# Performance work log

Hardware: AMD Instinct MI355X
Metric: run time of the kernel (lower is better)

Reference implementation:

```python
import jax, jax.numpy as jnp
import numpy as np

B = 524288
NF, NH1, NH21, NH22, NCLS = 5, 128, 32, 32, 1


def setup_inputs() -> dict:
    key = jax.random.key(0)
    ks = jax.random.split(key, 12)
    s = 0.05
    return {
        "x": jax.random.normal(ks[0], (B, NF), dtype=jnp.float32),
        "mean": jnp.zeros((NF,), dtype=jnp.float32),
        "std": jnp.ones((NF,), dtype=jnp.float32),
        "W1": jax.random.normal(ks[1], (NH1, NF), dtype=jnp.float32) * s,
        "b1": jax.random.normal(ks[2], (NH1,), dtype=jnp.float32) * s,
        "W21": jax.random.normal(ks[3], (NH21, NH1), dtype=jnp.float32) * s,
        "b21": jax.random.normal(ks[4], (NH21,), dtype=jnp.float32) * s,
        "W22": jax.random.normal(ks[5], (NH22, NH1), dtype=jnp.float32) * s,
        "b22": jax.random.normal(ks[6], (NH22,), dtype=jnp.float32) * s,
        "W31": jax.random.normal(ks[7], (NCLS, NH21), dtype=jnp.float32) * s,
        "b31": jax.random.normal(ks[8], (NCLS,), dtype=jnp.float32) * s,
        "W32": jax.random.normal(ks[9], (NCLS, NH22), dtype=jnp.float32) * s,
        "b32": jax.random.normal(ks[10], (NCLS,), dtype=jnp.float32) * s,
    }


def reference(x, mean, std, W1, b1, W21, b21, W22, b22, W31, b31, W32, b32):
    # de-normalized state used to build the CBF inequality
    x0 = x * std + mean  # [B, 5]
    h1 = jax.nn.relu(x @ W1.T + b1)         # [B, 128]  (bn=False path)
    x21 = jax.nn.relu(h1 @ W21.T + b21)     # [B, 32]
    x22 = jax.nn.relu(h1 @ W22.T + b22)     # [B, 32]
    x31 = x21 @ W31.T + b31                 # [B, 1]  QP linear term p
    x32 = 4.0 * jax.nn.sigmoid(x22 @ W32.T + b32)  # [B, 1]  learned penalty
    # h for the single inequality 1.8*u <= h
    h = (x0[:, 1] - x0[:, 3])[:, None] + x32 * (x0[:, 0] - x0[:, 2] - 1.8 * x0[:, 3])[:, None]
    # Closed-form 1-D QP: min 0.5 u^2 + x31*u  s.t. 1.8 u <= h
    u_unc = -x31
    u = jnp.where(1.8 * u_unc <= h, u_unc, h / 1.8)  # [B, 1]
    return u
```

## Files before the change

### kernel.cpp

```cpp
#include <hip/hip_runtime.h>
#include <hip/hip_bf16.h>
#include <math.h>
#include <string.h>

typedef __attribute__((ext_vector_type(8))) short bf16x8;
typedef __attribute__((ext_vector_type(4))) float f32x4;
typedef __attribute__((ext_vector_type(16))) float f32x16;
typedef __attribute__((ext_vector_type(4))) unsigned int u32x4;

#define BLK 256


__device__ __forceinline__ unsigned int rne_bf16_bits(float w) {
    unsigned int u = __builtin_bit_cast(unsigned int, w);
    u += 0x7fffu + ((u >> 16) & 1u);
    return u >> 16;
}
__device__ __forceinline__ float bf16_to_f32(unsigned int bits) {
    return __builtin_bit_cast(float, bits << 16);
}
__device__ __forceinline__ unsigned int pk_bf16(float lo, float hi) {
    __hip_bfloat162 bp = __float22bfloat162_rn(make_float2(lo, hi));
    unsigned int r; memcpy(&r, &bp, 4);
    return r;
}

__global__ void setup_kernel(const float* __restrict__ W1, const float* __restrict__ b1,
                             const float* __restrict__ W21, const float* __restrict__ W22,
                             unsigned short* __restrict__ w1f, unsigned short* __restrict__ frg)
{
    int t = blockIdx.x * blockDim.x + threadIdx.x;
    if (t < 2048) {
        int e = t;
        int tt = e >> 9, l = (e >> 3) & 63, j = e & 7;
        int n = tt * 32 + (l & 31), h = l >> 5;
        unsigned short v = 0;
        float src = 0.0f; bool have = false;
        if (j < 5)       { src = W1[n * 5 + j]; have = true; }
        else if (j == 5) { src = b1[n];         have = true; }
        if (have) {
            unsigned int hi = rne_bf16_bits(src);
            if (h == 0) v = (unsigned short)hi;
            else        v = (unsigned short)rne_bf16_bits(src - bf16_to_f32(hi));
        }
        w1f[e] = v;
    }
    for (int e = t; e < 16 * 64 * 8; e += 4096) {
        int F = e >> 9, l = (e >> 3) & 63, j = e & 7;
        int mat = F >> 3, kt = F & 7;
        int tt = kt >> 1, c = kt & 1;
        int n2 = l & 31, h = l >> 5;
        int k = 32 * tt + 16 * c + 4 * h + (j & 3) + 8 * (j >> 2);
        const float* W = mat ? W22 : W21;
        frg[e] = (unsigned short)rne_bf16_bits(W[n2 * 128 + k]);
    }
}

__global__ __launch_bounds__(BLK, 3) void barriernet_kernel(
    const float* __restrict__ x,
    const float* __restrict__ mean, const float* __restrict__ stdv,
    const float* __restrict__ b21, const float* __restrict__ b22,
    const float* __restrict__ W31, const float* __restrict__ b31,
    const float* __restrict__ W32, const float* __restrict__ b32,
    const u32x4* __restrict__ w1fg, const u32x4* __restrict__ frg,
    float* __restrict__ out, int zero)
{
    __shared__ u32x4 ldsF[1024];

    const int tid = threadIdx.x;
    #pragma unroll
    for (int i = 0; i < 4; ++i) ldsF[tid + i * BLK] = frg[tid + i * BLK];

    const int lane = tid & 63;
    const int wave = tid >> 6;
    const int R    = lane & 31;
    const int h    = lane >> 5;

    u32x4 w1f[4];
    #pragma unroll
    for (int t = 0; t < 4; ++t) w1f[t] = w1fg[t * 64 + lane];

    f32x4 bc21[4], bc22[4], wh31[4], wh32[4];
    #pragma unroll
    for (int rq = 0; rq < 4; ++rq) {
        bc21[rq] = *(const f32x4*)(b21 + 8 * rq + 4 * h);
        bc22[rq] = *(const f32x4*)(b22 + 8 * rq + 4 * h);
        wh31[rq] = *(const f32x4*)(W31 + 8 * rq + 4 * h);
        wh32[rq] = *(const f32x4*)(W32 + 8 * rq + 4 * h);
    }

    float sm_s[5], sm_m[5];
    #pragma unroll
    for (int f = 0; f < 5; ++f) { sm_s[f] = stdv[f]; sm_m[f] = mean[f]; }
    const float b31s = b31[0], b32s = b32[0];

    __syncthreads();

    const size_t wrow0 = (size_t)blockIdx.x * 512 + wave * 128;

    float4 xc4; float xc1;
    {
        const float* p = x + (wrow0 + R) * 5;
        xc4 = *(const float4*)p; xc1 = p[4];
    }

    #pragma unroll 1
    for (int it = 0; it < 4; ++it) {
        const int itn = (it < 3) ? it + 1 : 3;
        const float* pn = x + (wrow0 + itn * 32 + R) * 5;
        float4 xn4 = *(const float4*)pn;
        float  xn1 = pn[4];

        const float xf[5] = { xc4.x, xc4.y, xc4.z, xc4.w, xc1 };

        u32x4 xd;
        xd[0] = pk_bf16(xf[0], xf[1]);
        xd[1] = pk_bf16(xf[2], xf[3]);
        xd[2] = pk_bf16(xf[4], 1.0f);
        xd[3] = 0u;
        const bf16x8 xb = __builtin_bit_cast(bf16x8, xd);

        unsigned int au[8][4];
        #pragma unroll
        for (int t = 0; t < 4; ++t) {
            f32x16 z = {};
            f32x16 D = __builtin_amdgcn_mfma_f32_32x32x16_bf16(
                __builtin_bit_cast(bf16x8, w1f[t]), xb, z, 0, 0, 0);
            #pragma unroll
            for (int c = 0; c < 2; ++c)
                #pragma unroll
                for (int d = 0; d < 4; ++d)
                    au[2 * t + c][d] = pk_bf16(fmaxf(D[8 * c + 2 * d],     0.0f),
                                               fmaxf(D[8 * c + 2 * d + 1], 0.0f));
        }

        f32x16 acc21, acc22;
        #pragma unroll
        for (int rq = 0; rq < 4; ++rq)
            #pragma unroll
            for (int r = 0; r < 4; ++r) {
                acc21[rq * 4 + r] = bc21[rq][r];
                acc22[rq * 4 + r] = bc22[rq][r];
            }
        const int fz = it * zero;
        #pragma unroll
        for (int kt = 0; kt < 8; ++kt) {
            u32x4 t4 = { au[kt][0], au[kt][1], au[kt][2], au[kt][3] };
            const bf16x8 b = __builtin_bit_cast(bf16x8, t4);
            const bf16x8 wa21 = __builtin_bit_cast(bf16x8, ldsF[kt * 64 + lane + fz]);
            const bf16x8 wa22 = __builtin_bit_cast(bf16x8, ldsF[(8 + kt) * 64 + lane + fz]);
            acc21 = __builtin_amdgcn_mfma_f32_32x32x16_bf16(wa21, b, acc21, 0, 0, 0);
            acc22 = __builtin_amdgcn_mfma_f32_32x32x16_bf16(wa22, b, acc22, 0, 0, 0);
        }

        float s31 = 0.0f, s32 = 0.0f;
        #pragma unroll
        for (int rq = 0; rq < 4; ++rq)
            #pragma unroll
            for (int r = 0; r < 4; ++r) {
                s31 = fmaf(fmaxf(acc21[rq * 4 + r], 0.0f), wh31[rq][r], s31);
                s32 = fmaf(fmaxf(acc22[rq * 4 + r], 0.0f), wh32[rq][r], s32);
            }
        s31 += __shfl_xor(s31, 32);
        s32 += __shfl_xor(s32, 32);

        const float x31 = s31 + b31s;
        const float z   = s32 + b32s;
        const float x32 = 4.0f / (1.0f + __expf(-z));
        float x0[5];
        #pragma unroll
        for (int f = 0; f < 5; ++f) x0[f] = fmaf(xf[f], sm_s[f], sm_m[f]);
        const float h_ineq = (x0[1] - x0[3]) + x32 * (x0[0] - x0[2] - 1.8f * x0[3]);
        const float u_unc  = -x31;
        const float u      = (1.8f * u_unc <= h_ineq) ? u_unc : (h_ineq / 1.8f);
        if (lane < 32)
            out[wrow0 + it * 32 + R] = u;

        xc4 = xn4; xc1 = xn1;
    }
}

extern "C" void kernel_launch(void* const* d_in, const int* in_sizes, int n_in,
                              void* d_out, int out_size, void* d_ws, size_t ws_size,
                              hipStream_t stream) {
    const float* x    = (const float*)d_in[0];
    const float* mean = (const float*)d_in[1];
    const float* stdv = (const float*)d_in[2];
    const float* W1   = (const float*)d_in[3];
    const float* b1   = (const float*)d_in[4];
    const float* W21  = (const float*)d_in[5];
    const float* b21  = (const float*)d_in[6];
    const float* W22  = (const float*)d_in[7];
    const float* b22  = (const float*)d_in[8];
    const float* W31  = (const float*)d_in[9];
    const float* b31  = (const float*)d_in[10];
    const float* W32  = (const float*)d_in[11];
    const float* b32  = (const float*)d_in[12];
    float* out = (float*)d_out;

    unsigned short* w1f = (unsigned short*)d_ws;
    unsigned short* frg = (unsigned short*)((char*)d_ws + 4096);

    setup_kernel<<<16, 256, 0, stream>>>(W1, b1, W21, W22, w1f, frg);

    barriernet_kernel<<<1024, BLK, 0, stream>>>(
        x, mean, stdv, b21, b22, W31, b31, W32, b32,
        (const u32x4*)w1f, (const u32x4*)frg, out, 0);
}
```

Measured before the change: 102.7 us.

## Interleave layer-1 and layer-2 MFMAs and split accumulators to break dependency chains

Layer-2 MFMAs are now issued right after each layer-1 MFMA tile is converted to bf16, so packed activations are consumed immediately instead of being held for all eight k-tiles. The two layer-2 outputs each get two independent accumulator chains (even and odd k-tiles), which shortens the serial MFMA dependency. The final dot product is split into partial sums reduced as a tree. This adds accumulator registers, which could pressure occupancy under the 3-block launch bound.

```diff
diff --git a/kernel.cpp b/kernel.cpp
--- a/kernel.cpp
+++ b/kernel.cpp
@@ -120,53 +120,63 @@
         xd[3] = 0u;
         const bf16x8 xb = __builtin_bit_cast(bf16x8, xd);
 
-        unsigned int au[8][4];
+        f32x16 a21A, a21B, a22A, a22B;
+        #pragma unroll
+        for (int rq = 0; rq < 4; ++rq)
+            #pragma unroll
+            for (int r = 0; r < 4; ++r) {
+                a21A[rq * 4 + r] = bc21[rq][r];
+                a22A[rq * 4 + r] = bc22[rq][r];
+            }
+        const int fz = it * zero;
         #pragma unroll
         for (int t = 0; t < 4; ++t) {
             f32x16 z = {};
             f32x16 D = __builtin_amdgcn_mfma_f32_32x32x16_bf16(
                 __builtin_bit_cast(bf16x8, w1f[t]), xb, z, 0, 0, 0);
+            u32x4 au0, au1;
             #pragma unroll
-            for (int c = 0; c < 2; ++c)
-                #pragma unroll
-                for (int d = 0; d < 4; ++d)
-                    au[2 * t + c][d] = pk_bf16(fmaxf(D[8 * c + 2 * d],     0.0f),
-                                               fmaxf(D[8 * c + 2 * d + 1], 0.0f));
+            for (int d = 0; d < 4; ++d) {
+                au0[d] = pk_bf16(fmaxf(D[2 * d],     0.0f), fmaxf(D[2 * d + 1],     0.0f));
+                au1[d] = pk_bf16(fmaxf(D[8 + 2 * d], 0.0f), fmaxf(D[8 + 2 * d + 1], 0.0f));
+            }
+            const bf16x8 b0 = __builtin_bit_cast(bf16x8, au0);
+            const bf16x8 b1 = __builtin_bit_cast(bf16x8, au1);
+            const bf16x8 wa21e = __builtin_bit_cast(bf16x8, ldsF[(2 * t)     * 64 + lane + fz]);
+            const bf16x8 wa21o = __builtin_bit_cast(bf16x8, ldsF[(2 * t + 1) * 64 + lane + fz]);
+            const bf16x8 wa22e = __builtin_bit_cast(bf16x8, ldsF[(8 + 2 * t)     * 64 + lane + fz]);
+            const bf16x8 wa22o = __builtin_bit_cast(bf16x8, ldsF[(8 + 2 * t + 1) * 64 + lane + fz]);
+            a21A = __builtin_amdgcn_mfma_f32_32x32x16_bf16(wa21e, b0, a21A, 0, 0, 0);
+            a22A = __builtin_amdgcn_mfma_f32_32x32x16_bf16(wa22e, b0, a22A, 0, 0, 0);
+            if (t == 0) {
+                a21B = __builtin_amdgcn_mfma_f32_32x32x16_bf16(wa21o, b1, z, 0, 0, 0);
+                a22B = __builtin_amdgcn_mfma_f32_32x32x16_bf16(wa22o, b1, z, 0, 0, 0);
+            } else {
+                a21B = __builtin_amdgcn_mfma_f32_32x32x16_bf16(wa21o, b1, a21B, 0, 0, 0);
+                a22B = __builtin_amdgcn_mfma_f32_32x32x16_bf16(wa22o, b1, a22B, 0, 0, 0);
+            }
         }
 
-        f32x16 acc21, acc22;
-        #pragma unroll
-        for (int rq = 0; rq < 4; ++rq)
+        float p31[4], p32[4];
+        #pragma unroll
+        for (int rq = 0; rq < 4; ++rq) {
+            float q31 = 0.0f, q32 = 0.0f;
             #pragma unroll
             for (int r = 0; r < 4; ++r) {
-                acc21[rq * 4 + r] = bc21[rq][r];
-                acc22[rq * 4 + r] = bc22[rq][r];
-            }
-        const int fz = it * zero;
-        #pragma unroll
-        for (int kt = 0; kt < 8; ++kt) {
-            u32x4 t4 = { au[kt][0], au[kt][1], au[kt][2], au[kt][3] };
-            const bf16x8 b = __builtin_bit_cast(bf16x8, t4);
-            const bf16x8 wa21 = __builtin_bit_cast(bf16x8, ldsF[kt * 64 + lane + fz]);
-            const bf16x8 wa22 = __builtin_bit_cast(bf16x8, ldsF[(8 + kt) * 64 + lane + fz]);
-            acc21 = __builtin_amdgcn_mfma_f32_32x32x16_bf16(wa21, b, acc21, 0, 0, 0);
-            acc22 = __builtin_amdgcn_mfma_f32_32x32x16_bf16(wa22, b, acc22, 0, 0, 0);
+                const int i = rq * 4 + r;
+                q31 = fmaf(fmaxf(a21A[i] + a21B[i], 0.0f), wh31[rq][r], q31);
+                q32 = fmaf(fmaxf(a22A[i] + a22B[i], 0.0f), wh32[rq][r], q32);
+            }
+            p31[rq] = q31; p32[rq] = q32;
         }
-
-        float s31 = 0.0f, s32 = 0.0f;
-        #pragma unroll
-        for (int rq = 0; rq < 4; ++rq)
-            #pragma unroll
-            for (int r = 0; r < 4; ++r) {
-                s31 = fmaf(fmaxf(acc21[rq * 4 + r], 0.0f), wh31[rq][r], s31);
-                s32 = fmaf(fmaxf(acc22[rq * 4 + r], 0.0f), wh32[rq][r], s32);
-            }
+        float s31 = (p31[0] + p31[1]) + (p31[2] + p31[3]);
+        float s32 = (p32[0] + p32[1]) + (p32[2] + p32[3]);
         s31 += __shfl_xor(s31, 32);
         s32 += __shfl_xor(s32, 32);
 
         const float x31 = s31 + b31s;
-        const float z   = s32 + b32s;
-        const float x32 = 4.0f / (1.0f + __expf(-z));
+        const float z2  = s32 + b32s;
+        const float x32 = 4.0f / (1.0f + __expf(-z2));
         float x0[5];
         #pragma unroll
         for (int f = 0; f < 5; ++f) x0[f] = fmaf(xf[f], sm_s[f], sm_m[f]);
```

Result: slower. 107.9 us (+5.0%).
